# Performance work log

Hardware: AMD Instinct MI355X
Metric: run time of the kernel (lower is better)

The kernel has to match this reference:

```python
import jax, jax.numpy as jnp
import numpy as np

B, S, H = 2, 2048, 1024
NH, HD = 16, 64  # num_heads, head_dim
NEG = -1e9


def setup_inputs() -> dict:
    key = jax.random.key(0)
    ks = jax.random.split(key, 5)
    hidden_states = jax.random.normal(ks[0], (B, S, H), dtype=jnp.float32)
    # additive causal mask, broadcast over batch and heads
    causal = jnp.tril(jnp.ones((S, S), dtype=bool))
    attention_mask = jnp.where(causal, 0.0, NEG).astype(jnp.float32)[None, None]
    W_attn = jax.random.normal(ks[1], (H, 3 * H), dtype=jnp.float32) * 0.02
    b_attn = jax.random.normal(ks[2], (3 * H,), dtype=jnp.float32) * 0.02
    W_proj = jax.random.normal(ks[3], (H, H), dtype=jnp.float32) * 0.02
    b_proj = jax.random.normal(ks[4], (H,), dtype=jnp.float32) * 0.02
    return {"hidden_states": hidden_states, "attention_mask": attention_mask,
            "W_attn": W_attn, "b_attn": b_attn, "W_proj": W_proj, "b_proj": b_proj}


def reference(hidden_states, attention_mask, W_attn, b_attn, W_proj, b_proj):
    scale = HD ** -0.5
    # fused QKV projection: [B,S,3H]
    qkv = hidden_states @ W_attn + b_attn
    q, k, v = jnp.split(qkv, 3, axis=-1)
    # [B,S,H] -> [B,NH,S,HD]
    def heads(x):
        return x.reshape(B, S, NH, HD).transpose(0, 2, 1, 3)
    q, k, v = heads(q), heads(k), heads(v)
    # vanilla (prefill) attention: scores [B,NH,S,S]
    scores = jnp.einsum('bhqd,bhkd->bhqk', q, k) * scale + attention_mask
    probs = jax.nn.softmax(scores, axis=-1)
    ctx = jnp.einsum('bhqk,bhkd->bhqd', probs, v)
    # merge heads and output projection
    out = ctx.transpose(0, 2, 1, 3).reshape(B, S, H)
    return out @ W_proj + b_proj
```

## Files before the change

### kernel.cpp

```cpp
#include <hip/hip_runtime.h>
#include <hip/hip_bf16.h>

#define B_  2
#define S_  2048
#define H_  1024
#define NH_ 16
#define HD_ 64

typedef __attribute__((ext_vector_type(8))) short bf16x8;
typedef __attribute__((ext_vector_type(4))) float f32x4;
typedef __attribute__((ext_vector_type(4))) int   i32x4;

static __device__ __forceinline__ unsigned short f2bf(float f) {
    union { float f; unsigned int u; } v; v.f = f;
    unsigned int r = v.u + 0x7FFFu + ((v.u >> 16) & 1u);
    return (unsigned short)(r >> 16);
}
static __device__ __forceinline__ unsigned cvtpk(float a, float b) {
    unsigned r;
    asm("v_cvt_pk_bf16_f32 %0, %1, %2" : "=v"(r) : "v"(a), "v"(b));
    return r;
}

static __device__ __forceinline__ void barrier_keep_vmem() {
    __builtin_amdgcn_sched_barrier(0);
    asm volatile("s_waitcnt lgkmcnt(0)" ::: "memory");
    __builtin_amdgcn_s_barrier();
    __builtin_amdgcn_sched_barrier(0);
}
static __device__ __forceinline__ void barrier_exec_only() {
    __builtin_amdgcn_sched_barrier(0);
    __builtin_amdgcn_s_barrier();
    __builtin_amdgcn_sched_barrier(0);
}

__global__ __launch_bounds__(256) void prep_kernel(
    const float* __restrict__ hidden, unsigned short* __restrict__ hid_bf,
    const float* __restrict__ W_attn, unsigned short* __restrict__ wattn_t,
    const float* __restrict__ W_proj, unsigned short* __restrict__ wproj_t)
{
    __shared__ unsigned short t[64][65];
    const int bx = blockIdx.x, tid = threadIdx.x;
    if (bx < 4096) {
        int i = bx * 256 + tid;
        float4 v = ((const float4*)hidden)[i];
        ushort4 o;
        o.x = f2bf(v.x); o.y = f2bf(v.y); o.z = f2bf(v.z); o.w = f2bf(v.w);
        ((ushort4*)hid_bf)[i] = o;
        return;
    }
    const float* W; unsigned short* Wt; int K, N, n0, k0;
    if (bx < 4096 + 768) {
        const int ib = bx - 4096;
        W = W_attn; Wt = wattn_t; K = 1024; N = 3072;
        n0 = (ib % 48) * 64; k0 = (ib / 48) * 64;
    } else {
        const int ib = bx - 4096 - 768;
        W = W_proj; Wt = wproj_t; K = 1024; N = 1024;
        n0 = (ib % 16) * 64; k0 = (ib / 16) * 64;
    }
    #pragma unroll
    for (int i = 0; i < 16; ++i) {
        int idx = tid + i * 256; int r = idx >> 6, c = idx & 63;
        t[c][r] = f2bf(W[(size_t)(k0 + r) * N + n0 + c]);
    }
    __syncthreads();
    #pragma unroll
    for (int i = 0; i < 16; ++i) {
        int idx = tid + i * 256; int r = idx >> 6, c = idx & 63;
        Wt[(size_t)(n0 + r) * K + k0 + c] = t[r][c];
    }
}

template<int OUT_BF16>
__global__ __launch_bounds__(256) void gemm_mfma(
    const unsigned short* __restrict__ A,
    const unsigned short* __restrict__ Bt,
    const float* __restrict__ bias, void* __restrict__ Cv,
    int M, int N, int K)
{
    __shared__ __align__(16) unsigned short As[128][72];
    __shared__ __align__(16) unsigned short Bs[128][72];
    const int tid = threadIdx.x;
    const int lane = tid & 63, wave = tid >> 6;
    const int lr = lane & 15, lk = lane >> 4;
    const int wr = (wave >> 1) * 64, wc = (wave & 1) * 64;
    const int bm = blockIdx.y * 128, bn = blockIdx.x * 128;

    const int sr = tid >> 3;
    const int sc = (tid & 7) * 8;

    const unsigned short* pa = A  + (size_t)(bm + sr) * K + sc;
    const unsigned short* pb = Bt + (size_t)(bn + sr) * K + sc;

    i32x4 ra[4], rb[4];
    #pragma unroll
    for (int i = 0; i < 4; ++i) {
        ra[i] = *(const i32x4*)(pa + (size_t)(i * 32) * K);
        rb[i] = *(const i32x4*)(pb + (size_t)(i * 32) * K);
    }

    f32x4 acc[4][4];
    #pragma unroll
    for (int i = 0; i < 4; ++i)
        #pragma unroll
        for (int j = 0; j < 4; ++j)
            acc[i][j] = (f32x4){0.f, 0.f, 0.f, 0.f};

    for (int k0 = 0; k0 < K; k0 += 64) {
        #pragma unroll
        for (int i = 0; i < 4; ++i) {
            *(i32x4*)&As[sr + i * 32][sc] = ra[i];
            *(i32x4*)&Bs[sr + i * 32][sc] = rb[i];
        }
        barrier_keep_vmem();
        if (k0 + 64 < K) {
            #pragma unroll
            for (int i = 0; i < 4; ++i) {
                ra[i] = *(const i32x4*)(pa + (size_t)(i * 32) * K + k0 + 64);
                rb[i] = *(const i32x4*)(pb + (size_t)(i * 32) * K + k0 + 64);
            }
        }
        #pragma unroll
        for (int kk = 0; kk < 2; ++kk) {
            bf16x8 af[4], bfr[4];
            #pragma unroll
            for (int mi = 0; mi < 4; ++mi)
                af[mi] = *(const bf16x8*)&As[wr + mi * 16 + lr][kk * 32 + lk * 8];
            #pragma unroll
            for (int ni = 0; ni < 4; ++ni)
                bfr[ni] = *(const bf16x8*)&Bs[wc + ni * 16 + lr][kk * 32 + lk * 8];
            __builtin_amdgcn_s_setprio(1);
            #pragma unroll
            for (int mi = 0; mi < 4; ++mi)
                #pragma unroll
                for (int ni = 0; ni < 4; ++ni)
                    acc[mi][ni] = __builtin_amdgcn_mfma_f32_16x16x32_bf16(
                        af[mi], bfr[ni], acc[mi][ni], 0, 0, 0);
            __builtin_amdgcn_s_setprio(0);
        }
        barrier_exec_only();
    }

    #pragma unroll
    for (int ni = 0; ni < 4; ++ni) {
        const int col = bn + wc + ni * 16 + lr;
        const float bb = bias[col];
        #pragma unroll
        for (int mi = 0; mi < 4; ++mi) {
            #pragma unroll
            for (int r = 0; r < 4; ++r) {
                const int row = bm + wr + mi * 16 + lk * 4 + r;
                float v = acc[mi][ni][r] + bb;
                if (OUT_BF16)
                    ((unsigned short*)Cv)[(size_t)row * N + col] = f2bf(v);
                else
                    ((float*)Cv)[(size_t)row * N + col] = v;
            }
        }
    }
}

__global__ __launch_bounds__(512) void attn_mfma(
    const unsigned short* __restrict__ qkv, unsigned short* __restrict__ ctx)
{
    __shared__ __align__(16) unsigned short Ks[2][64][76];
    __shared__ __align__(16) unsigned short Vt[2][64][76];

    const int id   = blockIdx.x + 8 * (blockIdx.y + 16 * blockIdx.z);
    const int hb   = (id & 7) + 8 * ((id >> 3) & 3);
    const int pair = id >> 5;
    const int h = hb & 15, b = hb >> 4;

    const int tid = threadIdx.x, wave = tid >> 6, lane = tid & 63;
    const int lr = lane & 15, lk = lane >> 4;

    const int sr  = tid >> 3;
    const int scc = (tid & 7) * 8;
    const int rot = tid & 7;

    const float SC2  = 0.125f * 1.44269504089f;
    const float NM2C = -8.0f * 1.44269504089f;

    int buf = 0;
    #pragma unroll 1
    for (int half = 0; half < 2; ++half) {
        const int qt = half ? pair : (15 - pair);
        const int q0 = qt * 128;
        const int qW = q0 + wave * 16;
        const int qRow = qW + lr;
        const int nkt = 2 * qt + 2;

        const size_t qbase = (size_t)(b * S_ + qW + lr) * 3072 + h * 64;
        const bf16x8 qf0 = *(const bf16x8*)(qkv + qbase + lk * 8);
        const bf16x8 qf1 = *(const bf16x8*)(qkv + qbase + 32 + lk * 8);

        f32x4 oacc[4];
        #pragma unroll
        for (int d = 0; d < 4; ++d) oacc[d] = (f32x4){0.f, 0.f, 0.f, 0.f};
        float lpart = 0.0f;

        const size_t sbase = (size_t)(b * S_ + sr) * 3072 + h * 64 + scc;
        i32x4 kreg = *(const i32x4*)(qkv + sbase + 1024);
        i32x4 vreg = *(const i32x4*)(qkv + sbase + 2048);

        for (int kt = 0; kt < nkt; ++kt) {
            const int k0 = kt * 64;
            *(i32x4*)&Ks[buf][sr][scc] = kreg;
            {
                const unsigned short* vp = (const unsigned short*)&vreg;
                #pragma unroll
                for (int jj = 0; jj < 8; ++jj) {
                    const int j = (jj + rot) & 7;
                    Vt[buf][scc + j][sr] = vp[j];
                }
            }
            barrier_keep_vmem();
            if (kt + 1 < nkt) {
                const size_t nb = sbase + (size_t)(k0 + 64) * 3072;
                kreg = *(const i32x4*)(qkv + nb + 1024);
                vreg = *(const i32x4*)(qkv + nb + 2048);
            }

            if (k0 <= qW + 15) {
                f32x4 st[4];
                #pragma unroll
                for (int kb = 0; kb < 4; ++kb) st[kb] = (f32x4){0.f, 0.f, 0.f, 0.f};
                __builtin_amdgcn_s_setprio(1);
                #pragma unroll
                for (int kb = 0; kb < 4; ++kb) {
                    bf16x8 k0f = *(const bf16x8*)&Ks[buf][kb * 16 + lr][lk * 8];
                    bf16x8 k1f = *(const bf16x8*)&Ks[buf][kb * 16 + lr][32 + lk * 8];
                    st[kb] = __builtin_amdgcn_mfma_f32_16x16x32_bf16(k0f, qf0, st[kb], 0, 0, 0);
                    st[kb] = __builtin_amdgcn_mfma_f32_16x16x32_bf16(k1f, qf1, st[kb], 0, 0, 0);
                }
                __builtin_amdgcn_s_setprio(0);

                if (k0 + 63 > qW) {
                    #pragma unroll
                    for (int kb = 0; kb < 4; ++kb)
                        #pragma unroll
                        for (int r = 0; r < 4; ++r)
                            if (k0 + kb * 16 + lk * 4 + r > qRow) st[kb][r] = -3.0e38f;
                }

                unsigned pw[8];
                float psum = 0.0f;
                #pragma unroll
                for (int kb = 0; kb < 4; ++kb) {
                    float e0 = __builtin_amdgcn_exp2f(fmaf(st[kb][0], SC2, NM2C));
                    float e1 = __builtin_amdgcn_exp2f(fmaf(st[kb][1], SC2, NM2C));
                    float e2 = __builtin_amdgcn_exp2f(fmaf(st[kb][2], SC2, NM2C));
                    float e3 = __builtin_amdgcn_exp2f(fmaf(st[kb][3], SC2, NM2C));
                    psum += (e0 + e1) + (e2 + e3);
                    pw[kb * 2 + 0] = cvtpk(e0, e1);
                    pw[kb * 2 + 1] = cvtpk(e2, e3);
                }
                lpart += psum;

                const i32x4 pa0i = {(int)pw[0], (int)pw[1], (int)pw[2], (int)pw[3]};
                const i32x4 pa1i = {(int)pw[4], (int)pw[5], (int)pw[6], (int)pw[7]};
                const bf16x8 pa0 = __builtin_bit_cast(bf16x8, pa0i);
                const bf16x8 pa1 = __builtin_bit_cast(bf16x8, pa1i);

                __builtin_amdgcn_s_setprio(1);
                #pragma unroll
                for (int d = 0; d < 4; ++d) {
                    const int dc = d * 16 + lr;
                    uint2 lo0 = *(const uint2*)&Vt[buf][dc][4 * lk];
                    uint2 hi0 = *(const uint2*)&Vt[buf][dc][16 + 4 * lk];
                    uint2 lo1 = *(const uint2*)&Vt[buf][dc][32 + 4 * lk];
                    uint2 hi1 = *(const uint2*)&Vt[buf][dc][48 + 4 * lk];
                    const i32x4 v0i = {(int)lo0.x, (int)lo0.y, (int)hi0.x, (int)hi0.y};
                    const i32x4 v1i = {(int)lo1.x, (int)lo1.y, (int)hi1.x, (int)hi1.y};
                    const bf16x8 vb0 = __builtin_bit_cast(bf16x8, v0i);
                    const bf16x8 vb1 = __builtin_bit_cast(bf16x8, v1i);
                    oacc[d] = __builtin_amdgcn_mfma_f32_16x16x32_bf16(pa0, vb0, oacc[d], 0, 0, 0);
                    oacc[d] = __builtin_amdgcn_mfma_f32_16x16x32_bf16(pa1, vb1, oacc[d], 0, 0, 0);
                }
                __builtin_amdgcn_s_setprio(0);
            }
            buf ^= 1;
        }

        float l = lpart;
        l += __shfl_xor(l, 16);
        l += __shfl_xor(l, 32);
        const float linv = 1.0f / l;
        float iv[4];
        #pragma unroll
        for (int r = 0; r < 4; ++r)
            iv[r] = __shfl(linv, (lane & 48) | ((lane >> 2) & 12) | r);
        #pragma unroll
        for (int r = 0; r < 4; ++r) {
            const size_t orow = (size_t)(b * S_ + qW + lk * 4 + r) * 1024 + h * 64;
            #pragma unroll
            for (int d = 0; d < 4; ++d)
                ctx[orow + d * 16 + lr] = f2bf(oacc[d][r] * iv[r]);
        }
    }
}

extern "C" void kernel_launch(void* const* d_in, const int* in_sizes, int n_in,
                              void* d_out, int out_size, void* d_ws, size_t ws_size,
                              hipStream_t stream)
{
    const float* hidden = (const float*)d_in[0];
    const float* W_attn = (const float*)d_in[2];
    const float* b_attn = (const float*)d_in[3];
    const float* W_proj = (const float*)d_in[4];
    const float* b_proj = (const float*)d_in[5];
    float* out = (float*)d_out;

    unsigned short* hid_bf  = (unsigned short*)d_ws;
    unsigned short* wattn_t = hid_bf  + (size_t)4096 * 1024;
    unsigned short* wproj_t = wattn_t + (size_t)3072 * 1024;
    unsigned short* qkv     = wproj_t + (size_t)1024 * 1024;
    unsigned short* ctx     = qkv     + (size_t)4096 * 3072;

    prep_kernel<<<dim3(4096 + 768 + 256), 256, 0, stream>>>(
        hidden, hid_bf, W_attn, wattn_t, W_proj, wproj_t);

    gemm_mfma<1><<<dim3(3072 / 128, 4096 / 128), 256, 0, stream>>>(
        hid_bf, wattn_t, b_attn, qkv, 4096, 3072, 1024);

    attn_mfma<<<dim3(8, NH_, B_), 512, 0, stream>>>(qkv, ctx);

    gemm_mfma<0><<<dim3(1024 / 128, 4096 / 128), 256, 0, stream>>>(
        ctx, wproj_t, b_proj, out, 4096, 1024, 1024);
}
```

Before: 119.1 us.

## Switch attention to 32x32 MFMA tiles with split-K waves and LDS reduction

Rewrites the attention inner loop to use 32x32x16 bf16 MFMA. Waves are now split into two groups, each covering 32 queries and half of each 64-key tile, so the key dimension is divided across waves. The two groups' partial outputs and row sums are merged through LDS scratch that aliases the K/V buffers, with extra barriers before the write. The aim is fewer MFMA and LDS instructions per FLOP and a coarser causal skip. The cost is the reduction step, more registers per lane, and a tightened launch-bounds occupancy hint.

```diff
diff --git a/kernel.cpp b/kernel.cpp
--- a/kernel.cpp
+++ b/kernel.cpp
@@ -7,9 +7,10 @@
 #define NH_ 16
 #define HD_ 64
 
-typedef __attribute__((ext_vector_type(8))) short bf16x8;
-typedef __attribute__((ext_vector_type(4))) float f32x4;
-typedef __attribute__((ext_vector_type(4))) int   i32x4;
+typedef __attribute__((ext_vector_type(8)))  short bf16x8;
+typedef __attribute__((ext_vector_type(4)))  float f32x4;
+typedef __attribute__((ext_vector_type(16))) float f32x16;
+typedef __attribute__((ext_vector_type(4)))  int   i32x4;
 
 static __device__ __forceinline__ unsigned short f2bf(float f) {
     union { float f; unsigned int u; } v; v.f = f;
@@ -161,11 +162,14 @@
     }
 }
 
-__global__ __launch_bounds__(512) void attn_mfma(
+__global__ __launch_bounds__(512, 4) void attn_mfma(
     const unsigned short* __restrict__ qkv, unsigned short* __restrict__ ctx)
 {
-    __shared__ __align__(16) unsigned short Ks[2][64][76];
-    __shared__ __align__(16) unsigned short Vt[2][64][76];
+    __shared__ __align__(16) char lraw[38912];
+    unsigned short (*Ks)[64][76] = (unsigned short (*)[64][76])lraw;
+    unsigned short (*Vt)[64][76] = (unsigned short (*)[64][76])(lraw + 19456);
+    float (*scrO)[65] = (float (*)[65])lraw;
+    float* scrL = (float*)(lraw + 128 * 65 * 4);
 
     const int id   = blockIdx.x + 8 * (blockIdx.y + 16 * blockIdx.z);
     const int hb   = (id & 7) + 8 * ((id >> 3) & 3);
@@ -173,7 +177,8 @@
     const int h = hb & 15, b = hb >> 4;
 
     const int tid = threadIdx.x, wave = tid >> 6, lane = tid & 63;
-    const int lr = lane & 15, lk = lane >> 4;
+    const int lq = lane & 31, hi = lane >> 5;
+    const int g = wave >> 2, w4 = wave & 3;
 
     const int sr  = tid >> 3;
     const int scc = (tid & 7) * 8;
@@ -187,17 +192,19 @@
     for (int half = 0; half < 2; ++half) {
         const int qt = half ? pair : (15 - pair);
         const int q0 = qt * 128;
-        const int qW = q0 + wave * 16;
-        const int qRow = qW + lr;
+        const int qW = q0 + w4 * 32;
+        const int qRow = qW + lq;
         const int nkt = 2 * qt + 2;
 
-        const size_t qbase = (size_t)(b * S_ + qW + lr) * 3072 + h * 64;
-        const bf16x8 qf0 = *(const bf16x8*)(qkv + qbase + lk * 8);
-        const bf16x8 qf1 = *(const bf16x8*)(qkv + qbase + 32 + lk * 8);
-
-        f32x4 oacc[4];
-        #pragma unroll
-        for (int d = 0; d < 4; ++d) oacc[d] = (f32x4){0.f, 0.f, 0.f, 0.f};
+        const size_t qbase = (size_t)(b * S_ + qW + lq) * 3072 + h * 64;
+        bf16x8 qf[4];
+        #pragma unroll
+        for (int c = 0; c < 4; ++c)
+            qf[c] = *(const bf16x8*)(qkv + qbase + c * 16 + hi * 8);
+
+        f32x16 oacc[2];
+        #pragma unroll
+        for (int r = 0; r < 16; ++r) { oacc[0][r] = 0.f; oacc[1][r] = 0.f; }
         float lpart = 0.0f;
 
         const size_t sbase = (size_t)(b * S_ + sr) * 3072 + h * 64 + scc;
@@ -222,82 +229,86 @@
                 vreg = *(const i32x4*)(qkv + nb + 2048);
             }
 
-            if (k0 <= qW + 15) {
-                f32x4 st[4];
-                #pragma unroll
-                for (int kb = 0; kb < 4; ++kb) st[kb] = (f32x4){0.f, 0.f, 0.f, 0.f};
+            const int kbase = k0 + g * 32;
+            if (kbase <= qW + 31) {
+                f32x16 st;
+                #pragma unroll
+                for (int r = 0; r < 16; ++r) st[r] = 0.f;
                 __builtin_amdgcn_s_setprio(1);
                 #pragma unroll
-                for (int kb = 0; kb < 4; ++kb) {
-                    bf16x8 k0f = *(const bf16x8*)&Ks[buf][kb * 16 + lr][lk * 8];
-                    bf16x8 k1f = *(const bf16x8*)&Ks[buf][kb * 16 + lr][32 + lk * 8];
-                    st[kb] = __builtin_amdgcn_mfma_f32_16x16x32_bf16(k0f, qf0, st[kb], 0, 0, 0);
-                    st[kb] = __builtin_amdgcn_mfma_f32_16x16x32_bf16(k1f, qf1, st[kb], 0, 0, 0);
+                for (int c = 0; c < 4; ++c) {
+                    bf16x8 kf = *(const bf16x8*)&Ks[buf][g * 32 + lq][c * 16 + hi * 8];
+                    st = __builtin_amdgcn_mfma_f32_32x32x16_bf16(kf, qf[c], st, 0, 0, 0);
                 }
                 __builtin_amdgcn_s_setprio(0);
 
-                if (k0 + 63 > qW) {
+                if (kbase + 31 > qW) {
                     #pragma unroll
-                    for (int kb = 0; kb < 4; ++kb)
-                        #pragma unroll
-                        for (int r = 0; r < 4; ++r)
-                            if (k0 + kb * 16 + lk * 4 + r > qRow) st[kb][r] = -3.0e38f;
+                    for (int r = 0; r < 16; ++r)
+                        if (kbase + (r & 3) + 8 * (r >> 2) + 4 * hi > qRow)
+                            st[r] = -3.0e38f;
                 }
 
                 unsigned pw[8];
                 float psum = 0.0f;
                 #pragma unroll
-                for (int kb = 0; kb < 4; ++kb) {
-                    float e0 = __builtin_amdgcn_exp2f(fmaf(st[kb][0], SC2, NM2C));
-                    float e1 = __builtin_amdgcn_exp2f(fmaf(st[kb][1], SC2, NM2C));
-                    float e2 = __builtin_amdgcn_exp2f(fmaf(st[kb][2], SC2, NM2C));
-                    float e3 = __builtin_amdgcn_exp2f(fmaf(st[kb][3], SC2, NM2C));
-                    psum += (e0 + e1) + (e2 + e3);
-                    pw[kb * 2 + 0] = cvtpk(e0, e1);
-                    pw[kb * 2 + 1] = cvtpk(e2, e3);
+                for (int r2 = 0; r2 < 8; ++r2) {
+                    float e0 = __builtin_amdgcn_exp2f(fmaf(st[2 * r2],     SC2, NM2C));
+                    float e1 = __builtin_amdgcn_exp2f(fmaf(st[2 * r2 + 1], SC2, NM2C));
+                    psum += e0 + e1;
+                    pw[r2] = cvtpk(e0, e1);
                 }
                 lpart += psum;
 
-                const i32x4 pa0i = {(int)pw[0], (int)pw[1], (int)pw[2], (int)pw[3]};
-                const i32x4 pa1i = {(int)pw[4], (int)pw[5], (int)pw[6], (int)pw[7]};
-                const bf16x8 pa0 = __builtin_bit_cast(bf16x8, pa0i);
-                const bf16x8 pa1 = __builtin_bit_cast(bf16x8, pa1i);
-
                 __builtin_amdgcn_s_setprio(1);
                 #pragma unroll
-                for (int d = 0; d < 4; ++d) {
-                    const int dc = d * 16 + lr;
-                    uint2 lo0 = *(const uint2*)&Vt[buf][dc][4 * lk];
-                    uint2 hi0 = *(const uint2*)&Vt[buf][dc][16 + 4 * lk];
-                    uint2 lo1 = *(const uint2*)&Vt[buf][dc][32 + 4 * lk];
-                    uint2 hi1 = *(const uint2*)&Vt[buf][dc][48 + 4 * lk];
-                    const i32x4 v0i = {(int)lo0.x, (int)lo0.y, (int)hi0.x, (int)hi0.y};
-                    const i32x4 v1i = {(int)lo1.x, (int)lo1.y, (int)hi1.x, (int)hi1.y};
-                    const bf16x8 vb0 = __builtin_bit_cast(bf16x8, v0i);
-                    const bf16x8 vb1 = __builtin_bit_cast(bf16x8, v1i);
-                    oacc[d] = __builtin_amdgcn_mfma_f32_16x16x32_bf16(pa0, vb0, oacc[d], 0, 0, 0);
-                    oacc[d] = __builtin_amdgcn_mfma_f32_16x16x32_bf16(pa1, vb1, oacc[d], 0, 0, 0);
+                for (int kc = 0; kc < 2; ++kc) {
+                    const i32x4 pai = {(int)pw[4 * kc + 0], (int)pw[4 * kc + 1],
+                                       (int)pw[4 * kc + 2], (int)pw[4 * kc + 3]};
+                    const bf16x8 pa = __builtin_bit_cast(bf16x8, pai);
+                    const int base = g * 32 + kc * 16 + 4 * hi;
+                    #pragma unroll
+                    for (int db = 0; db < 2; ++db) {
+                        uint2 lo = *(const uint2*)&Vt[buf][db * 32 + lq][base];
+                        uint2 h2 = *(const uint2*)&Vt[buf][db * 32 + lq][base + 8];
+                        const i32x4 vi = {(int)lo.x, (int)lo.y, (int)h2.x, (int)h2.y};
+                        const bf16x8 vb = __builtin_bit_cast(bf16x8, vi);
+                        oacc[db] = __builtin_amdgcn_mfma_f32_32x32x16_bf16(pa, vb, oacc[db], 0, 0, 0);
+                    }
                 }
                 __builtin_amdgcn_s_setprio(0);
             }
             buf ^= 1;
         }
 
-        float l = lpart;
-        l += __shfl_xor(l, 16);
-        l += __shfl_xor(l, 32);
-        const float linv = 1.0f / l;
-        float iv[4];
-        #pragma unroll
-        for (int r = 0; r < 4; ++r)
-            iv[r] = __shfl(linv, (lane & 48) | ((lane >> 2) & 12) | r);
-        #pragma unroll
-        for (int r = 0; r < 4; ++r) {
-            const size_t orow = (size_t)(b * S_ + qW + lk * 4 + r) * 1024 + h * 64;
-            #pragma unroll
-            for (int d = 0; d < 4; ++d)
-                ctx[orow + d * 16 + lr] = f2bf(oacc[d][r] * iv[r]);
-        }
+        float lg = lpart + __shfl_xor(lpart, 32);
+
+        barrier_exec_only();
+        if (g == 1) {
+            #pragma unroll
+            for (int r = 0; r < 16; ++r) {
+                const int rowl = (r & 3) + 8 * (r >> 2) + 4 * hi;
+                scrO[w4 * 32 + rowl][lq]      = oacc[0][r];
+                scrO[w4 * 32 + rowl][32 + lq] = oacc[1][r];
+            }
+            if (hi == 0) scrL[w4 * 32 + lq] = lg;
+        }
+        barrier_exec_only();
+        if (g == 0) {
+            const float lB = scrL[w4 * 32 + lq];
+            const float linv = 1.0f / (lg + lB);
+            #pragma unroll
+            for (int r = 0; r < 16; ++r) {
+                const int rowl = (r & 3) + 8 * (r >> 2) + 4 * hi;
+                const float iv = __shfl(linv, rowl);
+                const size_t orow = (size_t)(b * S_ + qW + rowl) * 1024 + h * 64;
+                const float v0 = oacc[0][r] + scrO[w4 * 32 + rowl][lq];
+                const float v1 = oacc[1][r] + scrO[w4 * 32 + rowl][32 + lq];
+                ctx[orow + lq]      = f2bf(v0 * iv);
+                ctx[orow + 32 + lq] = f2bf(v1 * iv);
+            }
+        }
+        barrier_exec_only();
     }
 }
 
```

Measured after the change: 140.7 us. 18.2% more time.
